# Kernel optimization log

Hardware: AMD Instinct MI355X
Metric: run time of the kernel (lower is better)

The kernel has to match this reference:

```python
import jax, jax.numpy as jnp
import numpy as np

N_ENTITIES = 100000
N_USERS = 100000
N_ITEMS = 50000
N_ASPECTS = 64
CHANNEL = 64
N_EDGES = 1250000
N_RELATIONS = 16


def setup_inputs() -> dict:
    key = jax.random.key(0)
    ks = jax.random.split(key, 9)
    entity_emb = jax.random.normal(ks[0], (N_ENTITIES, CHANNEL), dtype=jnp.float32)
    item_emb = jax.random.normal(ks[1], (N_ITEMS, CHANNEL), dtype=jnp.float32)
    user_emb = jax.random.normal(ks[2], (N_USERS, CHANNEL), dtype=jnp.float32)
    aspect_emb = jax.random.normal(ks[3], (N_ASPECTS, CHANNEL), dtype=jnp.float32)
    edge_index = jax.random.randint(ks[4], (2, N_EDGES), 0, N_ENTITIES, dtype=jnp.int64)
    # edge_type values in [2, N_RELATIONS+2) since forward does weight[edge_type - 2]
    edge_type = jax.random.randint(ks[5], (N_EDGES,), 0, N_RELATIONS, dtype=jnp.int64) + 2
    # dense stand-ins for the sparse interaction matrices (n_aspects is small)
    ua_interact_mat = jax.random.uniform(ks[6], (N_USERS, N_ASPECTS), dtype=jnp.float32)
    ia_interact_mat = jax.random.uniform(ks[7], (N_ITEMS, N_ASPECTS), dtype=jnp.float32)
    weight = jax.random.normal(ks[8], (N_RELATIONS, CHANNEL), dtype=jnp.float32)
    return {
        "entity_emb": entity_emb, "item_emb": item_emb, "user_emb": user_emb,
        "aspect_emb": aspect_emb, "edge_index": edge_index, "edge_type": edge_type,
        "ua_interact_mat": ua_interact_mat, "ia_interact_mat": ia_interact_mat,
        "weight": weight,
    }


def reference(entity_emb, item_emb, user_emb, aspect_emb, edge_index, edge_type,
              ua_interact_mat, ia_interact_mat, weight):
    n_entities = entity_emb.shape[0]
    head, tail = edge_index[0], edge_index[1]

    # KG aggregate: gather tail entity + relation embeddings, multiply, scatter-mean by head
    edge_relation_emb = weight[edge_type - 2]          # [E, C]
    neigh_relation_emb = entity_emb[tail] * edge_relation_emb  # [E, C]
    sums = jax.ops.segment_sum(neigh_relation_emb, head, num_segments=n_entities)
    counts = jax.ops.segment_sum(jnp.ones(head.shape, dtype=neigh_relation_emb.dtype),
                                 head, num_segments=n_entities)
    entity_agg = sums / jnp.clip(counts, 1.0)[:, None]  # scatter_mean (0 where empty)

    # user->aspect attention (softmax over aspects; sum over aspect dim)
    score_ua = jax.nn.softmax(user_emb @ aspect_emb.T, axis=1)   # [U, A]
    score_ia = jax.nn.softmax(item_emb @ aspect_emb.T, axis=1)   # [I, A]

    user_agg = ua_interact_mat @ aspect_emb                      # [U, C]
    user_agg = user_agg * score_ua.sum(axis=1, keepdims=True) + user_agg

    item_agg = ia_interact_mat @ aspect_emb                      # [I, C]
    item_agg = item_agg * score_ia.sum(axis=1, keepdims=True) + item_agg

    return (item_agg, entity_agg, user_agg)
```

## Files before the change

kernel.cpp:

```cpp
#include <hip/hip_runtime.h>

#define N_EDGES   1250000
#define N_ENT     100000
#define N_USR     100000
#define N_ITM     50000
#define CH        64
#define CAP       48

#define ITEM_TILES ((N_ITM + 63) / 64)
#define USER_TILES ((N_USR + 63) / 64)
#define TOT_TILES  (ITEM_TILES + USER_TILES)

#define EPT 2
#define SCAT_BLKS ((N_EDGES + 256*EPT - 1) / (256*EPT))

__global__ __launch_bounds__(256, 4) void scatter_gemm_kernel(
    const int*   __restrict__ edge_index,
    const int*   __restrict__ edge_type,
    const float* __restrict__ aspect_emb,
    const float* __restrict__ ia_mat,
    const float* __restrict__ ua_mat,
    unsigned* __restrict__ cursor,
    unsigned* __restrict__ keys,
    float* __restrict__ out_item,
    float* __restrict__ out_user)
{
    {
        const int eA = blockIdx.x * (256 * EPT) + threadIdx.x;
        const int eB = eA + 256;
        const bool vA = (eA < N_EDGES);
        const bool vB = (eB < N_EDGES);
        const int la = vA ? eA : 0;
        const int lb = vB ? eB : 0;

        int headA = __builtin_nontemporal_load(&edge_index[la]);
        int headB = __builtin_nontemporal_load(&edge_index[lb]);
        int tailA = __builtin_nontemporal_load(&edge_index[N_EDGES + la]);
        int tailB = __builtin_nontemporal_load(&edge_index[N_EDGES + lb]);
        int relA  = __builtin_nontemporal_load(&edge_type[la]) - 2;
        int relB  = __builtin_nontemporal_load(&edge_type[lb]) - 2;

        unsigned posA = 0xFFFFFFFFu, posB = 0xFFFFFFFFu;
        if (vA) posA = atomicAdd(&cursor[headA], 1u);
        if (vB) posB = atomicAdd(&cursor[headB], 1u);

        if (vA && posA < CAP)
            keys[(unsigned)headA * CAP + posA] =
                (unsigned)tailA | ((unsigned)relA << 20);
        if (vB && posB < CAP)
            keys[(unsigned)headB * CAP + posB] =
                (unsigned)tailB | ((unsigned)relB << 20);
    }

    int tile = blockIdx.x;
    if (tile >= TOT_TILES) return;

    const float* M; float* out; int N, tt;
    if (tile < ITEM_TILES) { M = ia_mat; out = out_item; N = N_ITM; tt = tile; }
    else                   { M = ua_mat; out = out_user; N = N_USR; tt = tile - ITEM_TILES; }
    const int row0 = tt * 64;

    const int t  = threadIdx.x;
    const int ci = t & 15;
    const int r0 = (t >> 4) * 4;

    const float4* A4 = (const float4*)aspect_emb;
    const float4* M4 = (const float4*)M;

    int r[4];
    #pragma unroll
    for (int j = 0; j < 4; ++j) {
        int rr = row0 + r0 + j;
        r[j] = (rr < N) ? rr : (N - 1);
    }

    float4 acc[4];
    #pragma unroll
    for (int j = 0; j < 4; ++j) acc[j] = make_float4(0.f, 0.f, 0.f, 0.f);

    #pragma unroll 4
    for (int k4 = 0; k4 < 16; ++k4) {
        float4 a0 = A4[(k4 * 4 + 0) * 16 + ci];
        float4 a1 = A4[(k4 * 4 + 1) * 16 + ci];
        float4 a2 = A4[(k4 * 4 + 2) * 16 + ci];
        float4 a3 = A4[(k4 * 4 + 3) * 16 + ci];
        #pragma unroll
        for (int j = 0; j < 4; ++j) {
            float4 mv = M4[(size_t)r[j] * 16 + k4];
            acc[j].x += mv.x * a0.x + mv.y * a1.x + mv.z * a2.x + mv.w * a3.x;
            acc[j].y += mv.x * a0.y + mv.y * a1.y + mv.z * a2.y + mv.w * a3.y;
            acc[j].z += mv.x * a0.z + mv.y * a1.z + mv.z * a2.z + mv.w * a3.z;
            acc[j].w += mv.x * a0.w + mv.y * a1.w + mv.z * a2.w + mv.w * a3.w;
        }
    }

    float4* out4 = (float4*)out;
    #pragma unroll
    for (int j = 0; j < 4; ++j) {
        int rr = row0 + r0 + j;
        if (rr < N) {
            float4 v = acc[j];
            v.x *= 2.f; v.y *= 2.f; v.z *= 2.f; v.w *= 2.f;
            out4[(size_t)rr * 16 + ci] = v;
        }
    }
}

__global__ __launch_bounds__(256, 4) void reduce_kernel(
    const float* __restrict__ entity_emb,
    const float* __restrict__ weight,
    const unsigned* __restrict__ cursor,
    const unsigned* __restrict__ keys,
    float* __restrict__ out_ent)
{
    const int gtid = blockIdx.x * 256 + threadIdx.x;
    const int wave = gtid >> 6;
    const int lane = threadIdx.x & 63;
    const int half = lane >> 5;
    const int l32  = lane & 31;
    const int slot = l32 >> 3;
    const int q    = lane & 7;

    const int ent = wave * 2 + half;

    unsigned c = cursor[ent];
    if (c > CAP) c = CAP;
    const unsigned* bucket = keys + (unsigned)ent * CAP;

    const int nk = ((int)c > slot) ? (int)((c - (unsigned)slot + 3u) >> 2) : 0;

    unsigned kr[12];
    #pragma unroll
    for (int i = 0; i < 12; ++i)
        kr[i] = (i < nk) ? __builtin_nontemporal_load(&bucket[slot + 4 * i]) : 0u;

    const float4* emb4 = (const float4*)entity_emb;
    const float4* w4   = (const float4*)weight;

    float4 acc0 = make_float4(0.f, 0.f, 0.f, 0.f);
    float4 acc1 = make_float4(0.f, 0.f, 0.f, 0.f);

    #pragma unroll
    for (int i = 0; i < 12; ++i) {
        if (i < nk) {
            unsigned key  = kr[i];
            unsigned tail = key & 0xFFFFFu;
            unsigned rel  = key >> 20;
            const float4* ep = emb4 + (size_t)tail * 16 + q * 2;
            const float4* wp = w4 + rel * 16 + q * 2;
            float4 e0 = ep[0], e1 = ep[1];
            float4 w0 = wp[0], w1 = wp[1];
            acc0.x += e0.x * w0.x; acc0.y += e0.y * w0.y;
            acc0.z += e0.z * w0.z; acc0.w += e0.w * w0.w;
            acc1.x += e1.x * w1.x; acc1.y += e1.y * w1.y;
            acc1.z += e1.z * w1.z; acc1.w += e1.w * w1.w;
        }
    }

    #pragma unroll
    for (int off = 8; off <= 16; off <<= 1) {
        acc0.x += __shfl_xor(acc0.x, off); acc0.y += __shfl_xor(acc0.y, off);
        acc0.z += __shfl_xor(acc0.z, off); acc0.w += __shfl_xor(acc0.w, off);
        acc1.x += __shfl_xor(acc1.x, off); acc1.y += __shfl_xor(acc1.y, off);
        acc1.z += __shfl_xor(acc1.z, off); acc1.w += __shfl_xor(acc1.w, off);
    }

    if (slot == 0) {
        float inv = 1.0f / fmaxf((float)c, 1.0f);
        acc0.x *= inv; acc0.y *= inv; acc0.z *= inv; acc0.w *= inv;
        acc1.x *= inv; acc1.y *= inv; acc1.z *= inv; acc1.w *= inv;
        float4* o = (float4*)out_ent + (size_t)ent * 16 + q * 2;
        o[0] = acc0;
        o[1] = acc1;
    }
}

__global__ __launch_bounds__(256) void scatter_kernel(
    const float* __restrict__ entity_emb,
    const int* __restrict__ edge_index, const int* __restrict__ edge_type,
    const float* __restrict__ weight,
    float* __restrict__ ent_sum, float* __restrict__ cnt)
{
    int idx = blockIdx.x * 256 + threadIdx.x;
    int e = idx >> 4;
    int q = idx & 15;
    if (e >= N_EDGES) return;
    int head = edge_index[e];
    int tail = edge_index[N_EDGES + e];
    int rel  = edge_type[e] - 2;
    const float4* emb4 = (const float4*)entity_emb;
    const float4* w4   = (const float4*)weight;
    float4 ev = emb4[(size_t)tail * 16 + q];
    float4 wv = w4[rel * 16 + q];
    float* dst = ent_sum + (size_t)head * 64 + q * 4;
    atomicAdd(dst + 0, ev.x * wv.x);
    atomicAdd(dst + 1, ev.y * wv.y);
    atomicAdd(dst + 2, ev.z * wv.z);
    atomicAdd(dst + 3, ev.w * wv.w);
    if (q == 0) atomicAdd(&cnt[head], 1.0f);
}

__global__ __launch_bounds__(256) void divide_kernel(
    float* __restrict__ ent, const float* __restrict__ cnt)
{
    int idx = blockIdx.x * 256 + threadIdx.x;
    if (idx >= N_ENT * 16) return;
    int row = idx >> 4;
    float inv = 1.0f / fmaxf(cnt[row], 1.0f);
    float4* p = (float4*)ent;
    float4 v = p[idx];
    v.x *= inv; v.y *= inv; v.z *= inv; v.w *= inv;
    p[idx] = v;
}

__global__ __launch_bounds__(256) void gemm_fallback_kernel(
    const float* __restrict__ ia, const float* __restrict__ ua,
    const float* __restrict__ A,
    float* __restrict__ out_item, float* __restrict__ out_user)
{
    int tile = blockIdx.x;
    const float* M; float* out; int N, tt;
    if (tile < ITEM_TILES) { M = ia; out = out_item; N = N_ITM; tt = tile; }
    else                   { M = ua; out = out_user; N = N_USR; tt = tile - ITEM_TILES; }
    const int row0 = tt * 64;
    const int t  = threadIdx.x;
    const int ci = t & 15;
    const int r0 = (t >> 4) * 4;
    const float4* A4 = (const float4*)A;
    const float4* M4 = (const float4*)M;
    int r[4];
    #pragma unroll
    for (int j = 0; j < 4; ++j) {
        int rr = row0 + r0 + j;
        r[j] = (rr < N) ? rr : (N - 1);
    }
    float4 acc[4];
    #pragma unroll
    for (int j = 0; j < 4; ++j) acc[j] = make_float4(0.f, 0.f, 0.f, 0.f);
    #pragma unroll 4
    for (int k4 = 0; k4 < 16; ++k4) {
        float4 a0 = A4[(k4 * 4 + 0) * 16 + ci];
        float4 a1 = A4[(k4 * 4 + 1) * 16 + ci];
        float4 a2 = A4[(k4 * 4 + 2) * 16 + ci];
        float4 a3 = A4[(k4 * 4 + 3) * 16 + ci];
        #pragma unroll
        for (int j = 0; j < 4; ++j) {
            float4 mv = M4[(size_t)r[j] * 16 + k4];
            acc[j].x += mv.x * a0.x + mv.y * a1.x + mv.z * a2.x + mv.w * a3.x;
            acc[j].y += mv.x * a0.y + mv.y * a1.y + mv.z * a2.y + mv.w * a3.y;
            acc[j].z += mv.x * a0.z + mv.y * a1.z + mv.z * a2.z + mv.w * a3.z;
            acc[j].w += mv.x * a0.w + mv.y * a1.w + mv.z * a2.w + mv.w * a3.w;
        }
    }
    float4* out4 = (float4*)out;
    #pragma unroll
    for (int j = 0; j < 4; ++j) {
        int rr = row0 + r0 + j;
        if (rr < N) {
            float4 v = acc[j];
            v.x *= 2.f; v.y *= 2.f; v.z *= 2.f; v.w *= 2.f;
            out4[(size_t)rr * 16 + ci] = v;
        }
    }
}

extern "C" void kernel_launch(void* const* d_in, const int* in_sizes, int n_in,
                              void* d_out, int out_size, void* d_ws, size_t ws_size,
                              hipStream_t stream) {
    const float* entity_emb = (const float*)d_in[0];
    const float* aspect_emb = (const float*)d_in[3];
    const int*   edge_index = (const int*)d_in[4];
    const int*   edge_type  = (const int*)d_in[5];
    const float* ua_mat     = (const float*)d_in[6];
    const float* ia_mat     = (const float*)d_in[7];
    const float* weight     = (const float*)d_in[8];

    float* out_item = (float*)d_out;
    float* out_ent  = out_item + (size_t)N_ITM * CH;
    float* out_user = out_ent  + (size_t)N_ENT * CH;

    size_t need_fc = ((size_t)N_ENT + (size_t)N_ENT * CAP) * 4;

    if (ws_size >= need_fc) {
        unsigned* cursor = (unsigned*)d_ws;
        unsigned* keys   = cursor + N_ENT;

        (void)hipMemsetAsync(cursor, 0, (size_t)N_ENT * 4, stream);
        scatter_gemm_kernel<<<SCAT_BLKS, 256, 0, stream>>>(
            edge_index, edge_type, aspect_emb, ia_mat, ua_mat,
            cursor, keys, out_item, out_user);
        reduce_kernel<<<(N_ENT / 2) * 64 / 256, 256, 0, stream>>>(
            entity_emb, weight, cursor, keys, out_ent);
    } else {
        float* cnt = (float*)d_ws;
        (void)hipMemsetAsync(out_ent, 0, (size_t)N_ENT * CH * sizeof(float), stream);
        (void)hipMemsetAsync(cnt, 0, (size_t)N_ENT * sizeof(float), stream);
        scatter_kernel<<<(N_EDGES * 16 + 255) / 256, 256, 0, stream>>>(
            entity_emb, edge_index, edge_type, weight, out_ent, cnt);
        divide_kernel<<<(N_ENT * 16 + 255) / 256, 256, 0, stream>>>(out_ent, cnt);
        gemm_fallback_kernel<<<TOT_TILES, 256, 0, stream>>>(
            ia_mat, ua_mat, aspect_emb, out_item, out_user);
    }
}
```

Measured before the change: 305.9 us.

## Convert entity embeddings to bf16 and gather half-width rows in reduce

The scatter kernel now also converts entity_emb to a bf16 copy in workspace. A new reduce kernel gathers 128-byte bf16 tail rows instead of 256-byte fp32 rows and unpacks them to fp32 before the relation multiply and mean. This is meant to halve the bytes moved by the random gather that dominates the reduce. It costs an extra full pass over entity_emb (read fp32, write bf16) and adds bf16 rounding error to entity_agg.

```diff
diff --git a/kernel.cpp b/kernel.cpp
--- a/kernel.cpp
+++ b/kernel.cpp
@@ -14,14 +14,22 @@
 #define EPT 2
 #define SCAT_BLKS ((N_EDGES + 256*EPT - 1) / (256*EPT))
 
+__device__ __forceinline__ unsigned short bf16_rne(float f) {
+    unsigned u = __float_as_uint(f);
+    unsigned r = u + 0x7FFFu + ((u >> 16) & 1u);
+    return (unsigned short)(r >> 16);
+}
+
 __global__ __launch_bounds__(256, 4) void scatter_gemm_kernel(
     const int*   __restrict__ edge_index,
     const int*   __restrict__ edge_type,
+    const float* __restrict__ entity_emb,
     const float* __restrict__ aspect_emb,
     const float* __restrict__ ia_mat,
     const float* __restrict__ ua_mat,
     unsigned* __restrict__ cursor,
     unsigned* __restrict__ keys,
+    unsigned short* __restrict__ ent16,
     float* __restrict__ out_item,
     float* __restrict__ out_user)
 {
@@ -50,6 +58,20 @@
         if (vB && posB < CAP)
             keys[(unsigned)headB * CAP + posB] =
                 (unsigned)tailB | ((unsigned)relB << 20);
+    }
+
+    if (ent16) {
+        const int tid = blockIdx.x * 256 + threadIdx.x;
+        const int nth = SCAT_BLKS * 256;
+        const float4* src = (const float4*)entity_emb;
+        ushort4* dst = (ushort4*)ent16;
+        for (int g = tid; g < N_ENT * 16; g += nth) {
+            float4 v = src[g];
+            ushort4 o;
+            o.x = bf16_rne(v.x); o.y = bf16_rne(v.y);
+            o.z = bf16_rne(v.z); o.w = bf16_rne(v.w);
+            dst[g] = o;
+        }
     }
 
     int tile = blockIdx.x;
@@ -103,6 +125,82 @@
             v.x *= 2.f; v.y *= 2.f; v.z *= 2.f; v.w *= 2.f;
             out4[(size_t)rr * 16 + ci] = v;
         }
+    }
+}
+
+__global__ __launch_bounds__(256, 4) void reduce_bf16_kernel(
+    const unsigned short* __restrict__ ent16,
+    const float* __restrict__ weight,
+    const unsigned* __restrict__ cursor,
+    const unsigned* __restrict__ keys,
+    float* __restrict__ out_ent)
+{
+    const int gtid = blockIdx.x * 256 + threadIdx.x;
+    const int wave = gtid >> 6;
+    const int lane = threadIdx.x & 63;
+    const int half = lane >> 5;
+    const int l32  = lane & 31;
+    const int slot = l32 >> 3;
+    const int q    = lane & 7;
+
+    const int ent = wave * 2 + half;
+
+    unsigned c = cursor[ent];
+    if (c > CAP) c = CAP;
+    const unsigned* bucket = keys + (unsigned)ent * CAP;
+
+    const int nk = ((int)c > slot) ? (int)((c - (unsigned)slot + 3u) >> 2) : 0;
+
+    unsigned kr[12];
+    #pragma unroll
+    for (int i = 0; i < 12; ++i)
+        kr[i] = (i < nk) ? __builtin_nontemporal_load(&bucket[slot + 4 * i]) : 0u;
+
+    const uint4*  e16 = (const uint4*)ent16;
+    const float4* w4  = (const float4*)weight;
+
+    float4 acc0 = make_float4(0.f, 0.f, 0.f, 0.f);
+    float4 acc1 = make_float4(0.f, 0.f, 0.f, 0.f);
+
+    #pragma unroll
+    for (int i = 0; i < 12; ++i) {
+        if (i < nk) {
+            unsigned key  = kr[i];
+            unsigned tail = key & 0xFFFFFu;
+            unsigned rel  = key >> 20;
+            uint4 ev = e16[(size_t)tail * 8 + q];
+            const float4* wp = w4 + rel * 16 + q * 2;
+            float4 w0 = wp[0], w1 = wp[1];
+            float e0 = __uint_as_float(ev.x << 16);
+            float e1 = __uint_as_float(ev.x & 0xFFFF0000u);
+            float e2 = __uint_as_float(ev.y << 16);
+            float e3 = __uint_as_float(ev.y & 0xFFFF0000u);
+            float e4 = __uint_as_float(ev.z << 16);
+            float e5 = __uint_as_float(ev.z & 0xFFFF0000u);
+            float e6 = __uint_as_float(ev.w << 16);
+            float e7 = __uint_as_float(ev.w & 0xFFFF0000u);
+            acc0.x += e0 * w0.x; acc0.y += e1 * w0.y;
+            acc0.z += e2 * w0.z; acc0.w += e3 * w0.w;
+            acc1.x += e4 * w1.x; acc1.y += e5 * w1.y;
+            acc1.z += e6 * w1.z; acc1.w += e7 * w1.w;
+        }
+    }
+
+    #pragma unroll
+    for (int off = 8; off <= 16; off <<= 1) {
+        acc0.x += __shfl_xor(acc0.x, off); acc0.y += __shfl_xor(acc0.y, off);
+        acc0.z += __shfl_xor(acc0.z, off); acc0.w += __shfl_xor(acc0.w, off);
+        acc1.x += __shfl_xor(acc1.x, off); acc1.y += __shfl_xor(acc1.y, off);
+        acc1.z += __shfl_xor(acc1.z, off); acc1.w += __shfl_xor(acc1.w, off);
+    }
+
+    if (slot == 0) {
+        float inv = 1.0f / fmaxf((float)c, 1.0f);
+        acc0.x *= inv; acc0.y *= inv; acc0.z *= inv; acc0.w *= inv;
+        acc1.x *= inv; acc1.y *= inv; acc1.z *= inv; acc1.w *= inv;
+        float4* o = (float4*)out_ent + (size_t)ent * 16 + q * 2;
+        o[0] = acc0;
+        o[1] = acc1;
     }
 }
 
@@ -280,17 +378,25 @@
     float* out_user = out_ent  + (size_t)N_ENT * CH;
 
     size_t need_fc = ((size_t)N_ENT + (size_t)N_ENT * CAP) * 4;
+    size_t need_bf = need_fc + (size_t)N_ENT * CH * 2;
 
     if (ws_size >= need_fc) {
         unsigned* cursor = (unsigned*)d_ws;
         unsigned* keys   = cursor + N_ENT;
+        unsigned short* ent16 = (ws_size >= need_bf)
+            ? (unsigned short*)(keys + (size_t)N_ENT * CAP) : nullptr;
 
         (void)hipMemsetAsync(cursor, 0, (size_t)N_ENT * 4, stream);
         scatter_gemm_kernel<<<SCAT_BLKS, 256, 0, stream>>>(
-            edge_index, edge_type, aspect_emb, ia_mat, ua_mat,
-            cursor, keys, out_item, out_user);
-        reduce_kernel<<<(N_ENT / 2) * 64 / 256, 256, 0, stream>>>(
-            entity_emb, weight, cursor, keys, out_ent);
+            edge_index, edge_type, entity_emb, aspect_emb, ia_mat, ua_mat,
+            cursor, keys, ent16, out_item, out_user);
+        if (ent16) {
+            reduce_bf16_kernel<<<(N_ENT / 2) * 64 / 256, 256, 0, stream>>>(
+                ent16, weight, cursor, keys, out_ent);
+        } else {
+            reduce_kernel<<<(N_ENT / 2) * 64 / 256, 256, 0, stream>>>(
+                entity_emb, weight, cursor, keys, out_ent);
+        }
     } else {
         float* cnt = (float*)d_ws;
         (void)hipMemsetAsync(out_ent, 0, (size_t)N_ENT * CH * sizeof(float), stream);
```

New measurement: 299.4 us. -2.1%, faster.
